# Kernel optimization log

Measured on AMD Instinct MI355X. Metric: run time of the kernel, lower is better.

The kernel has to match this reference:

```python
import jax, jax.numpy as jnp
import numpy as np

EPS = 1e-6

def _conv(x, w, padding):
    # x: [B,C,H,W], w: [O,I,kh,kw]
    return jax.lax.conv_general_dilated(x, w, window_strides=(1, 1), padding=padding,
                                        dimension_numbers=('NCHW', 'OIHW', 'NCHW'))

def setup_inputs() -> dict:
    key = jax.random.key(0)
    ks = jax.random.split(key, 8)
    C = 512
    B, H, W = 4, 64, 64
    s1 = 1.0 / np.sqrt(C)          # 1x1 conv fan-in
    s3 = 1.0 / np.sqrt(C * 9)      # 3x3 conv fan-in
    return {
        'x': jax.random.normal(ks[0], (B, C, H, W), dtype=jnp.float32),
        'ln_w': jnp.ones((C,), dtype=jnp.float32),
        'ln_b': jnp.zeros((C,), dtype=jnp.float32),
        'wq': jax.random.normal(ks[1], (C, C, 1, 1), dtype=jnp.float32) * s1,
        'wk': jax.random.normal(ks[2], (C, C, 3, 3), dtype=jnp.float32) * s3,
        'wv': jax.random.normal(ks[3], (C, C, 3, 3), dtype=jnp.float32) * s3,
        'wp': jax.random.normal(ks[4], (C, C, 1, 1), dtype=jnp.float32) * s1,
        'bp': jnp.zeros((C,), dtype=jnp.float32),
    }

def reference(x, ln_w, ln_b, wq, wk, wv, wp, bp):
    # channels_first LayerNorm over C
    u = jnp.mean(x, axis=1, keepdims=True)
    s = jnp.mean((x - u) ** 2, axis=1, keepdims=True)
    h = (x - u) / jnp.sqrt(s + EPS)
    h = ln_w[None, :, None, None] * h + ln_b[None, :, None, None]

    q = _conv(h, wq, 'VALID')           # 1x1
    k = _conv(h, wk, [(1, 1), (1, 1)])  # 3x3, pad 1
    v = _conv(h, wv, [(1, 1), (1, 1)])

    b, c, H, W = q.shape
    hw = H * W
    q = q.reshape(b, c, hw)
    k = k.reshape(b, c, hw)
    v = v.reshape(b, c, hw)

    scale = jnp.asarray(int(c) ** (-0.5), q.dtype)
    attn = jnp.einsum('bcm,bcn->bmn', q, k) * scale  # [b, hw_q, hw_k]
    attn = jax.nn.softmax(attn, axis=2)
    out = jnp.einsum('bcn,bmn->bcm', v, attn)        # [b, c, hw_q]
    out = out.reshape(b, c, H, W)

    out = _conv(out, wp, 'VALID') + bp[None, :, None, None]
    return x + out
```

## Files before the change

### kernel.cpp

```cpp
#include <hip/hip_runtime.h>
#include <hip/hip_bf16.h>

#define C_DIM 512
#define HW    4096
#define BATCH 4
#define PW    66
#define PPIX  (PW*PW)

typedef __attribute__((ext_vector_type(8))) short bf16x8;
typedef __attribute__((ext_vector_type(4))) float f32x4;
typedef __attribute__((ext_vector_type(16))) float f32x16;
typedef __attribute__((ext_vector_type(2))) long long l64x2;

static __device__ __forceinline__ short f2b(float f) {
    union { float f; unsigned u; } v; v.f = f;
    unsigned r = v.u + 0x7fffu + ((v.u >> 16) & 1u);
    return (short)(r >> 16);
}
static __device__ __forceinline__ float b2f(short s) {
    union { unsigned u; float f; } v; v.u = ((unsigned)(unsigned short)s) << 16;
    return v.f;
}

static __device__ __forceinline__ f32x4 zero4() {
    f32x4 v = {0.f, 0.f, 0.f, 0.f};
    return v;
}
static __device__ __forceinline__ f32x16 zero16() {
    f32x16 v = {0.f,0.f,0.f,0.f, 0.f,0.f,0.f,0.f, 0.f,0.f,0.f,0.f, 0.f,0.f,0.f,0.f};
    return v;
}

static __device__ __forceinline__ void gload16(const void* g, void* l) {
    __builtin_amdgcn_global_load_lds(
        (__attribute__((address_space(1))) void*)g,
        (__attribute__((address_space(3))) void*)l, 16, 0, 0);
}

__global__ void k_cvt_bf16(const float* __restrict__ in, short* __restrict__ out, int n) {
    int i = blockIdx.x * 256 + threadIdx.x;
    if (i < n) out[i] = f2b(in[i]);
}

__global__ void k_reorder_w3(const float* __restrict__ w, short* __restrict__ out) {
    int i = blockIdx.x * 256 + threadIdx.x;
    int c   = i & 511;
    int tap = (i >> 9) % 9;
    int o   = i / (9 * 512);
    out[i] = f2b(w[((size_t)o * 512 + c) * 9 + tap]);
}

__global__ void k_cvt_k8(const short* __restrict__ in, unsigned char* __restrict__ out) {
    int i = blockIdx.x * 256 + threadIdx.x;
    int m = i >> 6;
    int p = (i & 63) * 8;
    int kcp = p >> 6, g = (p >> 4) & 3, half = (p >> 3) & 1;
    int chb = (kcp * 2 + half) * 32 + g * 8;
    bf16x8 v = *(const bf16x8*)&in[(size_t)m * 512 + chb];
    int lo = __builtin_amdgcn_cvt_pk_fp8_f32(b2f(v[0]), b2f(v[1]), 0, false);
    lo     = __builtin_amdgcn_cvt_pk_fp8_f32(b2f(v[2]), b2f(v[3]), lo, true);
    int hi = __builtin_amdgcn_cvt_pk_fp8_f32(b2f(v[4]), b2f(v[5]), 0, false);
    hi     = __builtin_amdgcn_cvt_pk_fp8_f32(b2f(v[6]), b2f(v[7]), hi, true);
    *(uint2*)&out[(size_t)m * 512 + p] = make_uint2((unsigned)lo, (unsigned)hi);
}

__global__ void k_ln_fused(const float* __restrict__ x, const float* __restrict__ lnw,
                           const float* __restrict__ lnb, short* __restrict__ hp) {
    __shared__ float red[8][64];
    __shared__ float mean_s[64], rstd_s[64];
    __shared__ short tile[64][65];
    int bid = blockIdx.x;
    int y = bid & 63, b = bid >> 6;
    int t = threadIdx.x;
    int px = t & 63, cg = t >> 6;
    const float* xb = x + (size_t)b * C_DIM * HW + (size_t)y * 64;

    float s = 0.f, sq = 0.f;
    for (int c = cg * 128; c < cg * 128 + 128; ++c) {
        float v = xb[(size_t)c * HW + px];
        s += v; sq += v * v;
    }
    red[cg][px] = s;
    red[4 + cg][px] = sq;
    __syncthreads();
    if (t < 64) {
        float S = red[0][t] + red[1][t] + red[2][t] + red[3][t];
        float Q = red[4][t] + red[5][t] + red[6][t] + red[7][t];
        float mu  = S * (1.0f / C_DIM);
        float var = Q * (1.0f / C_DIM) - mu * mu;
        mean_s[t] = mu;
        rstd_s[t] = 1.0f / sqrtf(var + 1e-6f);
    }
    __syncthreads();
    float mu = mean_s[px], rs = rstd_s[px];
    int cj = t & 63, pj = t >> 6;
    for (int ct = 0; ct < 8; ++ct) {
        int c0 = ct * 64;
        #pragma unroll
        for (int cc = 0; cc < 64; cc += 4) {
            int c = c0 + cc + cg;
            float v = xb[(size_t)c * HW + px];
            tile[cc + cg][px] = f2b((v - mu) * rs * lnw[c] + lnb[c]);
        }
        __syncthreads();
        #pragma unroll
        for (int pp = 0; pp < 64; pp += 4) {
            int pidx = pp + pj;
            size_t dst = ((size_t)b * PPIX + (size_t)(y + 1) * PW + 1 + pidx) * C_DIM + c0 + cj;
            hp[dst] = tile[cj][pidx];
        }
        __syncthreads();
    }
}

template<int TAPS, int GMODE, int EPI>
__global__ __launch_bounds__(256, 2) void k_gemm(
        const short* __restrict__ A, const short* __restrict__ Bw,
        void* __restrict__ Out, const float* __restrict__ bias,
        const float* __restrict__ resid)
{
    constexpr int K = TAPS * 512;
    constexpr int NKC = K / 64;
    __shared__ short Alds[128 * 64];
    __shared__ short Blds[128 * 64];
    int bid = blockIdx.x;
    int mt = bid & 31, nt = (bid >> 5) & 3, b = bid >> 7;
    int m0 = mt * 128, n0 = nt * 128;
    int t = threadIdx.x;
    int lane = t & 63, w = t >> 6;
    int wm = w >> 1, wn = w & 1;
    int g = lane >> 4, li = lane & 15;
    int srow = t >> 3, schunk = t & 7;
    const short* Ab = A + (GMODE == 0 ? (size_t)b * PPIX * C_DIM : (size_t)b * HW * C_DIM);

    f32x4 acc[4][4];
    #pragma unroll
    for (int i = 0; i < 4; ++i)
        #pragma unroll
        for (int j = 0; j < 4; ++j) acc[i][j] = zero4();

    for (int kc = 0; kc < NKC; ++kc) {
        int tap = (TAPS == 9) ? (kc >> 3) : 4;
        int cb  = (kc & 7) * 64;
        __syncthreads();
        #pragma unroll
        for (int r = 0; r < 4; ++r) {
            int row = r * 32 + srow;
            size_t goff;
            if (GMODE == 0) {
                int m = m0 + row;
                int yy = m >> 6, xx = m & 63;
                int pp = (yy + tap / 3) * PW + xx + (tap % 3);
                goff = (size_t)pp * C_DIM + cb + schunk * 8;
            } else {
                goff = (size_t)(m0 + row) * K + kc * 64 + schunk * 8;
            }
            gload16(Ab + goff, Alds + row * 64 + schunk * 8);
        }
        #pragma unroll
        for (int r = 0; r < 4; ++r) {
            int row = r * 32 + srow;
            size_t goff = (size_t)(n0 + row) * K + kc * 64 + schunk * 8;
            gload16(Bw + goff, Blds + row * 64 + schunk * 8);
        }
        __syncthreads();
        #pragma unroll
        for (int ks = 0; ks < 2; ++ks) {
            int koff = ks * 32 + g * 8;
            bf16x8 af[4], bfr[4];
            #pragma unroll
            for (int i = 0; i < 4; ++i)
                af[i] = *(const bf16x8*)&Alds[(wm * 64 + i * 16 + li) * 64 + koff];
            #pragma unroll
            for (int j = 0; j < 4; ++j)
                bfr[j] = *(const bf16x8*)&Blds[(wn * 64 + j * 16 + li) * 64 + koff];
            #pragma unroll
            for (int i = 0; i < 4; ++i)
                #pragma unroll
                for (int j = 0; j < 4; ++j)
                    acc[i][j] = __builtin_amdgcn_mfma_f32_16x16x32_bf16(af[i], bfr[j], acc[i][j], 0, 0, 0);
        }
    }
    #pragma unroll
    for (int fm = 0; fm < 4; ++fm) {
        #pragma unroll
        for (int fn = 0; fn < 4; ++fn) {
            int mrow = m0 + wm * 64 + fm * 16 + g * 4;
            int ncol = n0 + wn * 64 + fn * 16 + li;
            if constexpr (EPI == 0) {
                #pragma unroll
                for (int i = 0; i < 4; ++i) {
                    size_t dst = ((size_t)b * HW + mrow + i) * C_DIM + ncol;
                    ((short*)Out)[dst] = f2b(acc[fm][fn][i]);
                }
            } else if constexpr (EPI == 1) {
                size_t dst = ((size_t)b * C_DIM + ncol) * HW + mrow;
                short4 sv = make_short4(f2b(acc[fm][fn][0]), f2b(acc[fm][fn][1]),
                                        f2b(acc[fm][fn][2]), f2b(acc[fm][fn][3]));
                *(short4*)((short*)Out + dst) = sv;
            } else {
                size_t dst = ((size_t)b * C_DIM + ncol) * HW + mrow;
                float bb = bias[ncol];
                float4 xr = *(const float4*)(resid + dst);
                float4 o;
                o.x = acc[fm][fn][0] + bb + xr.x;
                o.y = acc[fm][fn][1] + bb + xr.y;
                o.z = acc[fm][fn][2] + bb + xr.z;
                o.w = acc[fm][fn][3] + bb + xr.w;
                *(float4*)((float*)Out + dst) = o;
            }
        }
    }
}

__global__ __launch_bounds__(256, 2) void k_gemm_kvq(
        const short* __restrict__ A, const short* __restrict__ Bk,
        const short* __restrict__ Bv, const short* __restrict__ Bq,
        short* __restrict__ OutK, short* __restrict__ OutV,
        short* __restrict__ OutQ)
{
    constexpr int K = 4608;
    __shared__ short Alds[128 * 64];
    __shared__ short Bklds[128 * 64];
    __shared__ short Bvlds[128 * 64];
    __shared__ short Bqlds[128 * 64];
    int bid0 = blockIdx.x;
    int bid = (bid0 & 7) * 64 + (bid0 >> 3);
    int mt = bid & 31, nt = (bid >> 5) & 3, b = bid >> 7;
    int m0 = mt * 128, n0 = nt * 128;
    int t = threadIdx.x;
    int lane = t & 63, w = t >> 6;
    int wm = w >> 1, wn = w & 1;
    int g = lane >> 4, li = lane & 15;
    int srow = t >> 3, schunk = t & 7;
    const short* Ab = A + (size_t)b * PPIX * C_DIM;

    f32x4 accK[4][4], accV[4][4], accQ[4][4];
    #pragma unroll
    for (int i = 0; i < 4; ++i)
        #pragma unroll
        for (int j = 0; j < 4; ++j) {
            accK[i][j] = zero4(); accV[i][j] = zero4(); accQ[i][j] = zero4();
        }

    for (int kc = 0; kc < 72; ++kc) {
        int tap = kc >> 3;
        int cb  = (kc & 7) * 64;
        bool qwin = (kc >= 32) && (kc < 40);
        __syncthreads();
        #pragma unroll
        for (int r = 0; r < 4; ++r) {
            int row = r * 32 + srow;
            int m = m0 + row;
            int yy = m >> 6, xx = m & 63;
            int pp = (yy + tap / 3) * PW + xx + (tap % 3);
            gload16(Ab + (size_t)pp * C_DIM + cb + schunk * 8, Alds + row * 64 + schunk * 8);
        }
        #pragma unroll
        for (int r = 0; r < 4; ++r) {
            int row = r * 32 + srow;
            size_t goff = (size_t)(n0 + row) * K + kc * 64 + schunk * 8;
            gload16(Bk + goff, Bklds + row * 64 + schunk * 8);
            gload16(Bv + goff, Bvlds + row * 64 + schunk * 8);
        }
        if (qwin) {
            #pragma unroll
            for (int r = 0; r < 4; ++r) {
                int row = r * 32 + srow;
                size_t goff = (size_t)(n0 + row) * 512 + (kc - 32) * 64 + schunk * 8;
                gload16(Bq + goff, Bqlds + row * 64 + schunk * 8);
            }
        }
        __syncthreads();
        #pragma unroll
        for (int ks = 0; ks < 2; ++ks) {
            int koff = ks * 32 + g * 8;
            bf16x8 af[4], bk[4], bv[4];
            #pragma unroll
            for (int i = 0; i < 4; ++i)
                af[i] = *(const bf16x8*)&Alds[(wm * 64 + i * 16 + li) * 64 + koff];
            #pragma unroll
            for (int j = 0; j < 4; ++j)
                bk[j] = *(const bf16x8*)&Bklds[(wn * 64 + j * 16 + li) * 64 + koff];
            #pragma unroll
            for (int i = 0; i < 4; ++i)
                #pragma unroll
                for (int j = 0; j < 4; ++j)
                    accK[i][j] = __builtin_amdgcn_mfma_f32_16x16x32_bf16(af[i], bk[j], accK[i][j], 0, 0, 0);
            #pragma unroll
            for (int j = 0; j < 4; ++j)
                bv[j] = *(const bf16x8*)&Bvlds[(wn * 64 + j * 16 + li) * 64 + koff];
            #pragma unroll
            for (int i = 0; i < 4; ++i)
                #pragma unroll
                for (int j = 0; j < 4; ++j)
                    accV[i][j] = __builtin_amdgcn_mfma_f32_16x16x32_bf16(af[i], bv[j], accV[i][j], 0, 0, 0);
            if (qwin) {
                #pragma unroll
                for (int j = 0; j < 4; ++j) {
                    bf16x8 bq = *(const bf16x8*)&Bqlds[(wn * 64 + j * 16 + li) * 64 + koff];
                    #pragma unroll
                    for (int i = 0; i < 4; ++i)
                        accQ[i][j] = __builtin_amdgcn_mfma_f32_16x16x32_bf16(af[i], bq, accQ[i][j], 0, 0, 0);
                }
            }
        }
    }
    #pragma unroll
    for (int fm = 0; fm < 4; ++fm) {
        #pragma unroll
        for (int fn = 0; fn < 4; ++fn) {
            int mrow = m0 + wm * 64 + fm * 16 + g * 4;
            int ncol = n0 + wn * 64 + fn * 16 + li;
            #pragma unroll
            for (int i = 0; i < 4; ++i) {
                size_t dst = ((size_t)b * HW + mrow + i) * C_DIM + ncol;
                OutK[dst] = f2b(accK[fm][fn][i]);
                OutQ[dst] = f2b(accQ[fm][fn][i]);
            }
            size_t dstv = ((size_t)b * C_DIM + ncol) * HW + mrow;
            short4 sv = make_short4(f2b(accV[fm][fn][0]), f2b(accV[fm][fn][1]),
                                    f2b(accV[fm][fn][2]), f2b(accV[fm][fn][3]));
            *(short4*)(OutV + dstv) = sv;
        }
    }
}

#define KT 32
#define NTILES 64
__global__ __launch_bounds__(512, 2) void k_attn(
        const short* __restrict__ qT, const unsigned char* __restrict__ kT8,
        const short* __restrict__ vg, short* __restrict__ O0,
        short* __restrict__ O1, float* __restrict__ L0, float* __restrict__ L1)
{
    __shared__ __align__(16) short pool[73728];
    unsigned char* Kp8 = (unsigned char*)pool;
    short* Vp = pool + 16384;
    short* Pp = pool + 57344;

    int bid0 = blockIdx.x;
    int bid = (bid0 & 7) * 32 + (bid0 >> 3);
    int qt = bid & 31, ks = (bid >> 5) & 1, b = bid >> 6;
    int m0 = qt * 128;
    int t = threadIdx.x, lane = t & 63, w = t >> 6;
    int g = lane >> 4, li = lane & 15;
    int l31 = lane & 31, l5 = lane >> 5;

    const unsigned char* kb8 = kT8 + ((size_t)b * HW + (size_t)ks * 2048) * 512;
    const short* vb = vg + (size_t)b * C_DIM * HW + ks * 2048;

    long long qf8[16];
    {
        const short* qrow = qT + ((size_t)b * HW + m0 + w * 16 + li) * C_DIM;
        #pragma unroll
        for (int kc = 0; kc < 16; ++kc) {
            bf16x8 qv = *(const bf16x8*)&qrow[kc * 32 + g * 8];
            int lo = __builtin_amdgcn_cvt_pk_fp8_f32(b2f(qv[0]), b2f(qv[1]), 0, false);
            lo     = __builtin_amdgcn_cvt_pk_fp8_f32(b2f(qv[2]), b2f(qv[3]), lo, true);
            int hi = __builtin_amdgcn_cvt_pk_fp8_f32(b2f(qv[4]), b2f(qv[5]), 0, false);
            hi     = __builtin_amdgcn_cvt_pk_fp8_f32(b2f(qv[6]), b2f(qv[7]), hi, true);
            qf8[kc] = ((long long)(unsigned)hi << 32) | (unsigned)lo;
        }
    }
    f32x16 oacc[8];
    #pragma unroll
    for (int a = 0; a < 8; ++a) oacc[a] = zero16();
    float lsum = 0.f;

    const unsigned char* ksrc8 = kb8 + (size_t)(t & 31) * 512 + (t >> 5) * 16;
    int voff[5];
    #pragma unroll
    for (int r = 0; r < 5; ++r) {
        int D = r * 512 + t;
        int ch = D / 5;
        int c  = D - ch * 5;
        voff[r] = (c < 4) ? ch * 4096 + c * 8 : 0;
    }

    const float SC = 0.044194173824159216f * 1.4426950408889634f;

    auto STAGE = [&](int buf, int nt) {
        int n0 = nt * KT;
        const unsigned char* kS = ksrc8 + (size_t)n0 * 512;
        unsigned char* kD = Kp8 + buf * 16384 + t * 16;
        gload16(kS, kD);
        gload16(kS + 256, kD + 8192);
        short* vD = Vp + buf * 20480 + t * 8;
        #pragma unroll
        for (int r = 0; r < 5; ++r)
            gload16(vb + voff[r] + n0, vD + r * 4096);
    };

    STAGE(0, 0);
    asm volatile("s_waitcnt vmcnt(0)" ::: "memory");
    __builtin_amdgcn_s_barrier();
    __builtin_amdgcn_sched_barrier(0);

    int buf = 0;
    for (int nt = 0; nt < NTILES; ++nt) {
        if (nt + 1 < NTILES) STAGE(buf ^ 1, nt + 1);

        const unsigned char* kbase8 = Kp8 + buf * 16384 + g * 512 + li * 16;
        f32x4 s0[2], s1[2];
        s0[0] = zero4(); s0[1] = zero4(); s1[0] = zero4(); s1[1] = zero4();
        __builtin_amdgcn_s_setprio(1);
        #pragma unroll
        for (int kcp = 0; kcp < 8; ++kcp) {
            #pragma unroll
            for (int fn = 0; fn < 2; ++fn) {
                l64x2 kv = *(const l64x2*)&kbase8[kcp * 2048 + fn * 256];
                s0[fn] = __builtin_amdgcn_mfma_f32_16x16x32_fp8_fp8(kv[0], qf8[2 * kcp],     s0[fn], 0, 0, 0);
                s1[fn] = __builtin_amdgcn_mfma_f32_16x16x32_fp8_fp8(kv[1], qf8[2 * kcp + 1], s1[fn], 0, 0, 0);
            }
        }
        __builtin_amdgcn_s_setprio(0);
        #pragma unroll
        for (int fn = 0; fn < 2; ++fn) {
            float e0 = exp2f((s0[fn][0] + s1[fn][0]) * SC);
            float e1 = exp2f((s0[fn][1] + s1[fn][1]) * SC);
            float e2 = exp2f((s0[fn][2] + s1[fn][2]) * SC);
            float e3 = exp2f((s0[fn][3] + s1[fn][3]) * SC);
            lsum += (e0 + e1) + (e2 + e3);
            union { __hip_bfloat162 h; unsigned u; } p01, p23;
            p01.h = __float22bfloat162_rn(make_float2(e0, e1));
            p23.h = __float22bfloat162_rn(make_float2(e2, e3));
            *(uint2*)&Pp[(w * 16 + li) * 40 + fn * 16 + g * 4] = make_uint2(p01.u, p23.u);
        }

        asm volatile("s_waitcnt lgkmcnt(0)" ::: "memory");
        __builtin_amdgcn_s_barrier();
        __builtin_amdgcn_sched_barrier(0);

        const short* vbase = Vp + buf * 20480 + (size_t)w * 64 * 40;
        bf16x8 vf[2][2];
        #pragma unroll
        for (int cht = 0; cht < 2; ++cht)
            #pragma unroll
            for (int kx = 0; kx < 2; ++kx)
                vf[cht][kx] = *(const bf16x8*)&vbase[(cht * 32 + l31) * 40 + kx * 16 + l5 * 8];
        __builtin_amdgcn_s_setprio(1);
        #pragma unroll
        for (int q2 = 0; q2 < 4; ++q2) {
            #pragma unroll
            for (int kx = 0; kx < 2; ++kx) {
                bf16x8 pf = *(const bf16x8*)&Pp[(q2 * 32 + l31) * 40 + kx * 16 + l5 * 8];
                oacc[q2 * 2 + 0] = __builtin_amdgcn_mfma_f32_32x32x16_bf16(vf[0][kx], pf, oacc[q2 * 2 + 0], 0, 0, 0);
                oacc[q2 * 2 + 1] = __builtin_amdgcn_mfma_f32_32x32x16_bf16(vf[1][kx], pf, oacc[q2 * 2 + 1], 0, 0, 0);
            }
        }
        __builtin_amdgcn_s_setprio(0);

        asm volatile("s_waitcnt vmcnt(0)" ::: "memory");
        __builtin_amdgcn_s_barrier();
        __builtin_amdgcn_sched_barrier(0);
        buf ^= 1;
    }

    lsum += __shfl_xor(lsum, 16);
    lsum += __shfl_xor(lsum, 32);
    float* Lb = (ks ? L1 : L0) + (size_t)b * HW + m0 + w * 16;
    if (lane < 16) Lb[lane] = lsum;

    short* tp = pool + w * 9216;
    #pragma unroll
    for (int a = 0; a < 8; ++a) {
        int q2 = a >> 1, cht = a & 1;
        int q_l = q2 * 32 + l31;
        #pragma unroll
        for (int rq = 0; rq < 4; ++rq) {
            int chb = cht * 32 + rq * 8 + l5 * 4;
            union { __hip_bfloat162 h; unsigned u; } x01, x23;
            x01.h = __float22bfloat162_rn(make_float2(oacc[a][rq * 4 + 0], oacc[a][rq * 4 + 1]));
            x23.h = __float22bfloat162_rn(make_float2(oacc[a][rq * 4 + 2], oacc[a][rq * 4 + 3]));
            *(uint2*)&tp[q_l * 72 + chb] = make_uint2(x01.u, x23.u);
        }
    }
    asm volatile("s_waitcnt lgkmcnt(0)" ::: "memory");
    __builtin_amdgcn_sched_barrier(0);
    short* Ob = (ks ? O1 : O0) + ((size_t)b * HW + m0) * C_DIM + w * 64;
    #pragma unroll
    for (int qg = 0; qg < 16; ++qg) {
        int qr = qg * 8 + (lane >> 3);
        bf16x8 v = *(const bf16x8*)&tp[qr * 72 + (lane & 7) * 8];
        *(bf16x8*)&Ob[(size_t)qr * C_DIM + (lane & 7) * 8] = v;
    }
}

__global__ void k_att_comb(const short* __restrict__ O0, const short* __restrict__ O1,
                           const float* __restrict__ L0, const float* __restrict__ L1,
                           short* __restrict__ oatt) {
    int i = blockIdx.x * 256 + threadIdx.x;
    int row = i >> 6;
    int c0 = (i & 63) * 8;
    float r = 1.0f / (L0[row] + L1[row]);
    size_t base = (size_t)row * C_DIM + c0;
    bf16x8 a = *(const bf16x8*)&O0[base];
    bf16x8 c = *(const bf16x8*)&O1[base];
    bf16x8 o;
    #pragma unroll
    for (int j = 0; j < 8; ++j)
        o[j] = f2b((b2f(a[j]) + b2f(c[j])) * r);
    *(bf16x8*)&oatt[base] = o;
}

extern "C" void kernel_launch(void* const* d_in, const int* in_sizes, int n_in,
                              void* d_out, int out_size, void* d_ws, size_t ws_size,
                              hipStream_t stream) {
    const float* x    = (const float*)d_in[0];
    const float* ln_w = (const float*)d_in[1];
    const float* ln_b = (const float*)d_in[2];
    const float* wq   = (const float*)d_in[3];
    const float* wk   = (const float*)d_in[4];
    const float* wv   = (const float*)d_in[5];
    const float* wp   = (const float*)d_in[6];
    const float* bp   = (const float*)d_in[7];
    float* out = (float*)d_out;

    char* ws = (char*)d_ws;
    size_t off = 0;
    auto alloc = [&](size_t bytes) {
        char* p = ws + off;
        off += (bytes + 255) & ~(size_t)255;
        return p;
    };
    short* hp   = (short*)alloc((size_t)BATCH * PPIX * C_DIM * 2);
    short* wqb  = (short*)alloc((size_t)512 * 512 * 2);
    short* wkr  = (short*)alloc((size_t)512 * 4608 * 2);
    short* wvr  = (short*)alloc((size_t)512 * 4608 * 2);
    short* wpb  = (short*)alloc((size_t)512 * 512 * 2);
    short* qT   = (short*)alloc((size_t)BATCH * HW * C_DIM * 2);
    short* kT   = (short*)alloc((size_t)BATCH * HW * C_DIM * 2);
    short* vg   = (short*)alloc((size_t)BATCH * HW * C_DIM * 2);
    short* oatt = (short*)alloc((size_t)BATCH * HW * C_DIM * 2);
    float* mean = (float*)alloc((size_t)BATCH * HW * 4);
    float* rstd = (float*)alloc((size_t)BATCH * HW * 4);

    hipMemsetAsync(hp, 0, (size_t)BATCH * PPIX * C_DIM * 2, stream);
    k_cvt_bf16<<<1024, 256, 0, stream>>>(wq, wqb, 512 * 512);
    k_cvt_bf16<<<1024, 256, 0, stream>>>(wp, wpb, 512 * 512);
    k_reorder_w3<<<9216, 256, 0, stream>>>(wk, wkr);
    k_reorder_w3<<<9216, 256, 0, stream>>>(wv, wvr);
    k_ln_fused<<<256, 256, 0, stream>>>(x, ln_w, ln_b, hp);

    k_gemm_kvq<<<512, 256, 0, stream>>>(hp, wkr, wvr, wqb, kT, vg, qT);

    unsigned char* kT8 = (unsigned char*)wkr;
    k_cvt_k8<<<4096, 256, 0, stream>>>(kT, kT8);

    short* Op0 = hp;
    short* Op1 = oatt;
    float* Ls0 = mean;
    float* Ls1 = rstd;
    k_attn<<<256, 512, 0, stream>>>(qT, kT8, vg, Op0, Op1, Ls0, Ls1);
    k_att_comb<<<4096, 256, 0, stream>>>(Op0, Op1, Ls0, Ls1, oatt);

    k_gemm<1, 1, 2><<<512, 256, 0, stream>>>(oatt, wpb, out, bp, x);
}
```

Before: 387.0 us.

## Split Q projection out of fused KVQ GEMM and double-buffer K/V GEMM

The Q 1x1 projection moves out of the fused K/V/Q conv GEMM into the existing generic k_gemm kernel. The K/V kernel becomes double-buffered with 32-wide K chunks and a padded LDS row stride of 40, so the next chunk's global loads overlap with MFMA work and there is one barrier per step. This drops the fourth LDS buffer, the Q accumulators and the block-index swizzle. The cost is an extra kernel launch and a second read of the LN output for Q, plus twice as many loop iterations and barriers.

```diff
diff --git a/kernel.cpp b/kernel.cpp
--- a/kernel.cpp
+++ b/kernel.cpp
@@ -213,99 +213,94 @@
     }
 }
 
-__global__ __launch_bounds__(256, 2) void k_gemm_kvq(
+__global__ __launch_bounds__(256, 2) void k_gemm_kv2(
         const short* __restrict__ A, const short* __restrict__ Bk,
-        const short* __restrict__ Bv, const short* __restrict__ Bq,
-        short* __restrict__ OutK, short* __restrict__ OutV,
-        short* __restrict__ OutQ)
+        const short* __restrict__ Bv, short* __restrict__ OutK,
+        short* __restrict__ OutV)
 {
     constexpr int K = 4608;
-    __shared__ short Alds[128 * 64];
-    __shared__ short Bklds[128 * 64];
-    __shared__ short Bvlds[128 * 64];
-    __shared__ short Bqlds[128 * 64];
-    int bid0 = blockIdx.x;
-    int bid = (bid0 & 7) * 64 + (bid0 >> 3);
+    __shared__ short Alds[2][5120];
+    __shared__ short Bklds[2][5120];
+    __shared__ short Bvlds[2][5120];
+    int bid = blockIdx.x;
     int mt = bid & 31, nt = (bid >> 5) & 3, b = bid >> 7;
     int m0 = mt * 128, n0 = nt * 128;
     int t = threadIdx.x;
     int lane = t & 63, w = t >> 6;
     int wm = w >> 1, wn = w & 1;
     int g = lane >> 4, li = lane & 15;
-    int srow = t >> 3, schunk = t & 7;
     const short* Ab = A + (size_t)b * PPIX * C_DIM;
 
-    f32x4 accK[4][4], accV[4][4], accQ[4][4];
+    int srowv[3], schv[3];
+    #pragma unroll
+    for (int r = 0; r < 3; ++r) {
+        int slot = r * 256 + t;
+        int row = slot / 5;
+        int ch = slot - row * 5;
+        srowv[r] = row;
+        schv[r] = (ch < 4) ? ch * 8 : 0;
+    }
+    bool act2 = (w < 2);
+
+    f32x4 accK[4][4], accV[4][4];
     #pragma unroll
     for (int i = 0; i < 4; ++i)
         #pragma unroll
-        for (int j = 0; j < 4; ++j) {
-            accK[i][j] = zero4(); accV[i][j] = zero4(); accQ[i][j] = zero4();
-        }
-
-    for (int kc = 0; kc < 72; ++kc) {
-        int tap = kc >> 3;
-        int cb  = (kc & 7) * 64;
-        bool qwin = (kc >= 32) && (kc < 40);
+        for (int j = 0; j < 4; ++j) { accK[i][j] = zero4(); accV[i][j] = zero4(); }
+
+    auto STAGE = [&](int bf, int kc2) {
+        int tap = kc2 >> 4;
+        int cofs = (kc2 & 15) * 32;
+        int ty3 = tap / 3, tx3 = tap % 3;
+        #pragma unroll
+        for (int r = 0; r < 3; ++r) {
+            if (r < 2 || act2) {
+                int row = srowv[r];
+                int m = m0 + row;
+                int yy = m >> 6, xx = m & 63;
+                int pp = (yy + ty3) * PW + xx + tx3;
+                int dst = (r * 256 + t) * 8;
+                gload16(Ab + (size_t)pp * C_DIM + cofs + schv[r], &Alds[bf][dst]);
+                size_t gb = (size_t)(n0 + row) * K + tap * 512 + cofs + schv[r];
+                gload16(Bk + gb, &Bklds[bf][dst]);
+                gload16(Bv + gb, &Bvlds[bf][dst]);
+            }
+        }
+    };
+
+    auto COMPUTE = [&](int bf) {
+        bf16x8 af[4], bk[4], bv[4];
+        #pragma unroll
+        for (int i = 0; i < 4; ++i)
+            af[i] = *(const bf16x8*)&Alds[bf][(wm * 64 + i * 16 + li) * 40 + g * 8];
+        #pragma unroll
+        for (int j = 0; j < 4; ++j)
+            bk[j] = *(const bf16x8*)&Bklds[bf][(wn * 64 + j * 16 + li) * 40 + g * 8];
+        #pragma unroll
+        for (int i = 0; i < 4; ++i)
+            #pragma unroll
+            for (int j = 0; j < 4; ++j)
+                accK[i][j] = __builtin_amdgcn_mfma_f32_16x16x32_bf16(af[i], bk[j], accK[i][j], 0, 0, 0);
+        #pragma unroll
+        for (int j = 0; j < 4; ++j)
+            bv[j] = *(const bf16x8*)&Bvlds[bf][(wn * 64 + j * 16 + li) * 40 + g * 8];
+        #pragma unroll
+        for (int i = 0; i < 4; ++i)
+            #pragma unroll
+            for (int j = 0; j < 4; ++j)
+                accV[i][j] = __builtin_amdgcn_mfma_f32_16x16x32_bf16(af[i], bv[j], accV[i][j], 0, 0, 0);
+    };
+
+    STAGE(0, 0);
+    __syncthreads();
+    int bf = 0;
+    for (int kc2 = 0; kc2 < 144; ++kc2) {
+        if (kc2 + 1 < 144) STAGE(bf ^ 1, kc2 + 1);
+        COMPUTE(bf);
         __syncthreads();
-        #pragma unroll
-        for (int r = 0; r < 4; ++r) {
-            int row = r * 32 + srow;
-            int m = m0 + row;
-            int yy = m >> 6, xx = m & 63;
-            int pp = (yy + tap / 3) * PW + xx + (tap % 3);
-            gload16(Ab + (size_t)pp * C_DIM + cb + schunk * 8, Alds + row * 64 + schunk * 8);
-        }
-        #pragma unroll
-        for (int r = 0; r < 4; ++r) {
-            int row = r * 32 + srow;
-            size_t goff = (size_t)(n0 + row) * K + kc * 64 + schunk * 8;
-            gload16(Bk + goff, Bklds + row * 64 + schunk * 8);
-            gload16(Bv + goff, Bvlds + row * 64 + schunk * 8);
-        }
-        if (qwin) {
-            #pragma unroll
-            for (int r = 0; r < 4; ++r) {
-                int row = r * 32 + srow;
-                size_t goff = (size_t)(n0 + row) * 512 + (kc - 32) * 64 + schunk * 8;
-                gload16(Bq + goff, Bqlds + row * 64 + schunk * 8);
-            }
-        }
-        __syncthreads();
-        #pragma unroll
-        for (int ks = 0; ks < 2; ++ks) {
-            int koff = ks * 32 + g * 8;
-            bf16x8 af[4], bk[4], bv[4];
-            #pragma unroll
-            for (int i = 0; i < 4; ++i)
-                af[i] = *(const bf16x8*)&Alds[(wm * 64 + i * 16 + li) * 64 + koff];
-            #pragma unroll
-            for (int j = 0; j < 4; ++j)
-                bk[j] = *(const bf16x8*)&Bklds[(wn * 64 + j * 16 + li) * 64 + koff];
-            #pragma unroll
-            for (int i = 0; i < 4; ++i)
-                #pragma unroll
-                for (int j = 0; j < 4; ++j)
-                    accK[i][j] = __builtin_amdgcn_mfma_f32_16x16x32_bf16(af[i], bk[j], accK[i][j], 0, 0, 0);
-            #pragma unroll
-            for (int j = 0; j < 4; ++j)
-                bv[j] = *(const bf16x8*)&Bvlds[(wn * 64 + j * 16 + li) * 64 + koff];
-            #pragma unroll
-            for (int i = 0; i < 4; ++i)
-                #pragma unroll
-                for (int j = 0; j < 4; ++j)
-                    accV[i][j] = __builtin_amdgcn_mfma_f32_16x16x32_bf16(af[i], bv[j], accV[i][j], 0, 0, 0);
-            if (qwin) {
-                #pragma unroll
-                for (int j = 0; j < 4; ++j) {
-                    bf16x8 bq = *(const bf16x8*)&Bqlds[(wn * 64 + j * 16 + li) * 64 + koff];
-                    #pragma unroll
-                    for (int i = 0; i < 4; ++i)
-                        accQ[i][j] = __builtin_amdgcn_mfma_f32_16x16x32_bf16(af[i], bq, accQ[i][j], 0, 0, 0);
-                }
-            }
-        }
-    }
+        bf ^= 1;
+    }
+
     #pragma unroll
     for (int fm = 0; fm < 4; ++fm) {
         #pragma unroll
@@ -316,7 +311,6 @@
             for (int i = 0; i < 4; ++i) {
                 size_t dst = ((size_t)b * HW + mrow + i) * C_DIM + ncol;
                 OutK[dst] = f2b(accK[fm][fn][i]);
-                OutQ[dst] = f2b(accQ[fm][fn][i]);
             }
             size_t dstv = ((size_t)b * C_DIM + ncol) * HW + mrow;
             short4 sv = make_short4(f2b(accV[fm][fn][0]), f2b(accV[fm][fn][1]),
@@ -542,7 +536,8 @@
     k_reorder_w3<<<9216, 256, 0, stream>>>(wv, wvr);
     k_ln_fused<<<256, 256, 0, stream>>>(x, ln_w, ln_b, hp);
 
-    k_gemm_kvq<<<512, 256, 0, stream>>>(hp, wkr, wvr, wqb, kT, vg, qT);
+    k_gemm<1, 0, 0><<<512, 256, 0, stream>>>(hp, wqb, qT, nullptr, nullptr);
+    k_gemm_kv2<<<512, 256, 0, stream>>>(hp, wkr, wvr, kT, vg);
 
     unsigned char* kT8 = (unsigned char*)wkr;
     k_cvt_k8<<<4096, 256, 0, stream>>>(kT, kT8);
```

After: 393.8 us. Within noise of the previous version (+1.7%).
